# Performance work log

Measured on AMD Instinct MI355X. Metric: run time of the kernel, lower is better.

## Reference

```python
import jax, jax.numpy as jnp
import numpy as np

B, T, D_MODEL, HEAD_SIZE = 8, 1024, 1024, 64
BLOCK_SIZE = 1024  # == max_relative_pos


def setup_inputs() -> dict:
    key = jax.random.key(0)
    ks = jax.random.split(key, 7)
    s = 1.0 / np.sqrt(D_MODEL)
    return {
        "x": jax.random.normal(ks[0], (B, T, D_MODEL), dtype=jnp.float32),
        "Wk": jax.random.normal(ks[1], (D_MODEL, HEAD_SIZE), dtype=jnp.float32) * s,
        "bk": jax.random.normal(ks[2], (HEAD_SIZE,), dtype=jnp.float32) * 0.02,
        "Wq": jax.random.normal(ks[3], (D_MODEL, HEAD_SIZE), dtype=jnp.float32) * s,
        "bq": jax.random.normal(ks[4], (HEAD_SIZE,), dtype=jnp.float32) * 0.02,
        "Wv": jax.random.normal(ks[5], (D_MODEL, HEAD_SIZE), dtype=jnp.float32) * s,
        "rel_emb": jax.random.normal(ks[6], (2 * BLOCK_SIZE + 1, HEAD_SIZE), dtype=jnp.float32) * 0.02,
        "mask": 1,
    }


def reference(x, Wk, bk, Wq, bq, Wv, rel_emb, mask):
    Bb, Tt, _ = x.shape
    hs = Wk.shape[1]
    max_rel = (rel_emb.shape[0] - 1) // 2

    k = x @ Wk + bk          # [B,T,hs]
    q = x @ Wq + bq          # [B,T,hs]
    v = x @ Wv               # [B,T,hs]

    pos = jnp.arange(Tt)
    idx = jnp.clip(pos[:, None] - pos[None, :], -max_rel, max_rel) + max_rel
    r = rel_emb[idx]         # [T,T,hs], r[i,j] = emb(clip(i-j))

    # scores[b,i,j] = (q[b,i] + r[i,j]) . (k[b,j] + r[j,i]) / sqrt(hs)
    scale = 1.0 / np.sqrt(hs).astype(np.float32)
    scores = (
        jnp.einsum("bid,bjd->bij", q, k)
        + jnp.einsum("bid,jid->bij", q, r)   # q_i . r[j,i]
        + jnp.einsum("ijd,bjd->bij", r, k)   # r[i,j] . k_j
        + jnp.einsum("ijd,jid->ij", r, r)[None]  # r[i,j] . r[j,i]
    ) * scale

    if mask:  # static Python int -> causal mask, matches tril masked_fill
        causal = jnp.tril(jnp.ones((Tt, Tt), dtype=bool))
        scores = jnp.where(causal, scores, jnp.float32(-jnp.inf))

    w = jax.nn.softmax(scores, axis=-1)  # dropout is identity in eval mode
    return w @ v  # [B,T,hs]
```

## Files before the change

### kernel.cpp

```cpp
#include <hip/hip_runtime.h>
#include <hip/hip_bf16.h>
#include <math.h>


typedef __hip_bfloat16 bf16;
typedef __attribute__((ext_vector_type(8))) short short8;
typedef __attribute__((ext_vector_type(4))) float f32x4;

#define NTRI 136
#define MFMA16(a, b, c) __builtin_amdgcn_mfma_f32_16x16x32_bf16(a, b, c, 0, 0, 0)

__device__ __forceinline__ float bf2f(bf16 h) { return __bfloat162float(h); }
__device__ __forceinline__ bf16 f2bf(float f) { return __float2bfloat16(f); }
__device__ __forceinline__ short bfs(float f) {
  bf16 h = __float2bfloat16(f);
  return *(short*)&h;
}

union U16 {
  uint4 u;
  short8 s;
};
__device__ __forceinline__ short8 ldfrag(const bf16* p) {
  U16 x;
  x.u = *(const uint4*)p;
  return x.s;
}

__global__ __launch_bounds__(256) void prep_kernel(
    const float* __restrict__ Wk, const float* __restrict__ Wq, const float* __restrict__ Wv,
    const float* __restrict__ E, bf16* __restrict__ WT, bf16* __restrict__ Ep,
    bf16* __restrict__ Erev, float* __restrict__ rrG) {
  const int bid = blockIdx.x, t = threadIdx.x;
  if (bid < 768) {
    int idx = bid * 256 + t;
    int sel = idx >> 16, r = idx & 65535;
    int n = r >> 10, kk = r & 1023;
    const float* W = (sel == 0) ? Wk : (sel == 1) ? Wq : Wv;
    WT[idx] = f2bf(W[kk * 64 + n]);
  } else if (bid < 1281) {
    int idx = (bid - 768) * 256 + t;
    if (idx < 2049 * 64) {
      int tt = idx >> 6, d = idx & 63;
      Ep[idx] = f2bf(E[idx]);
      Erev[idx] = f2bf(E[(2048 - tt) * 64 + d]);
    }
  } else {
    int dlt = ((bid - 1281) << 2) + (t >> 6);
    int d = t & 63;
    float p = E[(size_t)(1024 + dlt) * 64 + d] * E[(size_t)(1024 - dlt) * 64 + d];
#pragma unroll
    for (int off = 32; off > 0; off >>= 1) p += __shfl_down(p, off);
    if (d == 0) rrG[64 + dlt] = p;
  }
}

__global__ __launch_bounds__(256, 2) void qkv_mfma(
    const float* __restrict__ x, const bf16* __restrict__ WT,
    const float* __restrict__ bk, const float* __restrict__ bq,
    bf16* __restrict__ qB, bf16* __restrict__ kB, bf16* __restrict__ vT) {
  const int R0 = blockIdx.x << 4;
  const int t = threadIdx.x;
  const int lane = t & 63, wave = t >> 6;
  const int m = lane & 15, quad = lane >> 4;

  __shared__ float RED[4][16][196];
  __shared__ bf16 VTS[64][24];

  const float* xrow = x + (size_t)(R0 + m) * 1024 + (wave << 8);
  f32x4 acc[3][4];
#pragma unroll
  for (int s = 0; s < 3; ++s)
#pragma unroll
    for (int c = 0; c < 4; ++c) acc[s][c] = (f32x4){0.f, 0.f, 0.f, 0.f};

#pragma unroll
  for (int ks = 0; ks < 8; ++ks) {
    const int k0 = ks * 32 + quad * 8;
    float4 xa = *(const float4*)(xrow + k0);
    float4 xb = *(const float4*)(xrow + k0 + 4);
    short8 a;
    a[0] = bfs(xa.x); a[1] = bfs(xa.y); a[2] = bfs(xa.z); a[3] = bfs(xa.w);
    a[4] = bfs(xb.x); a[5] = bfs(xb.y); a[6] = bfs(xb.z); a[7] = bfs(xb.w);
    const int kg = (wave << 8) + k0;
#pragma unroll
    for (int sel = 0; sel < 3; ++sel)
#pragma unroll
      for (int ct = 0; ct < 4; ++ct) {
        const bf16* bb = WT + ((size_t)(sel * 64 + ct * 16 + m) << 10) + kg;
        acc[sel][ct] = MFMA16(a, ldfrag(bb), acc[sel][ct]);
      }
  }

#pragma unroll
  for (int sel = 0; sel < 3; ++sel)
#pragma unroll
    for (int ct = 0; ct < 4; ++ct)
#pragma unroll
      for (int r = 0; r < 4; ++r)
        RED[wave][quad * 4 + r][sel * 64 + ct * 16 + m] = acc[sel][ct][r];
  __syncthreads();

#pragma unroll
  for (int e = 0; e < 12; ++e) {
    int idx = e * 256 + t;
    int row = idx / 192, c = idx - row * 192;
    float s = RED[0][row][c] + RED[1][row][c] + RED[2][row][c] + RED[3][row][c];
    int sel = c >> 6, col = c & 63;
    size_t grow = (size_t)(R0 + row);
    if (sel == 0) kB[grow * 64 + col] = f2bf(s + bk[col]);
    else if (sel == 1) qB[grow * 64 + col] = f2bf(s + bq[col]);
    else VTS[col][row] = f2bf(s);
  }
  __syncthreads();
  {
    int dd = t >> 2, h = (t & 3) << 2;
    int b = R0 >> 10, tloc = R0 & 1023;
    *(uint2*)(vT + ((size_t)((b << 6) + dd) << 10) + tloc + h) = *(const uint2*)&VTS[dd][h];
  }
}

__global__ __launch_bounds__(256, 3) void flash_mfma(
    const bf16* __restrict__ qB, const bf16* __restrict__ kB, const bf16* __restrict__ vT,
    const bf16* __restrict__ Ep, const bf16* __restrict__ Erev, const float* __restrict__ rrG,
    float* __restrict__ ml, float* __restrict__ Opart) {
  const int bx = blockIdx.x;
  const int b = bx / NTRI;
  const int rr_ = bx - b * NTRI;
  int it = (int)((sqrtf(8.f * rr_ + 1.f) - 1.f) * 0.5f);
  while ((it + 1) * (it + 2) / 2 <= rr_) ++it;
  while (it * (it + 1) / 2 > rr_) --it;
  const int jt = rr_ - it * (it + 1) / 2;
  const int I0 = it << 6, J0 = jt << 6;
  const int D = I0 - J0, w0 = D - 64;
  const int slot = bx;

  const int t = threadIdx.x;
  const int lane = t & 63, wave = t >> 6;
  const int m = lane & 15, quad = lane >> 4;
  const int strip = wave << 4;

  __shared__ __align__(16) bf16 M2S[64][136];
  __shared__ bf16 M3S[64][136];
  bf16 (*PS)[80] = (bf16(*)[80])M2S;

  const bf16* qbase = qB + ((size_t)((b << 10) + I0 + strip + m) << 6);
  const short8 aq0 = ldfrag(qbase + quad * 8);
  const short8 aq1 = ldfrag(qbase + 32 + quad * 8);
  const bf16* kbase = kB + ((size_t)((b << 10) + J0 + strip + m) << 6);
  const short8 ak0 = ldfrag(kbase + quad * 8);
  const short8 ak1 = ldfrag(kbase + 32 + quad * 8);

  const bf16* erb = Erev + ((size_t)(1024 + w0) << 6);
#pragma unroll
  for (int ct = 0; ct < 8; ++ct) {
    const bf16* bb = erb + ((size_t)(ct * 16 + m) << 6) + quad * 8;
    const float rv = rrG[64 + w0 + ct * 16 + m];
    f32x4 c = (f32x4){0.f, 0.f, 0.f, 0.f};
    c = MFMA16(aq0, ldfrag(bb), c);
    c = MFMA16(aq1, ldfrag(bb + 32), c);
#pragma unroll
    for (int r = 0; r < 4; ++r) M2S[strip + quad * 4 + r][ct * 16 + m] = f2bf(c[r] + rv);
  }
  const bf16* epb = Ep + ((size_t)(1024 + w0) << 6);
#pragma unroll
  for (int ct = 0; ct < 8; ++ct) {
    const bf16* bb = epb + ((size_t)(ct * 16 + m) << 6) + quad * 8;
    f32x4 c = (f32x4){0.f, 0.f, 0.f, 0.f};
    c = MFMA16(ak0, ldfrag(bb), c);
    c = MFMA16(ak1, ldfrag(bb + 32), c);
#pragma unroll
    for (int r = 0; r < 4; ++r) M3S[strip + quad * 4 + r][ct * 16 + m] = f2bf(c[r]);
  }
  f32x4 acc[4];
#pragma unroll
  for (int ct = 0; ct < 4; ++ct) {
    const bf16* bb = kB + ((size_t)((b << 10) + J0 + ct * 16 + m) << 6) + quad * 8;
    f32x4 c = (f32x4){0.f, 0.f, 0.f, 0.f};
    c = MFMA16(aq0, ldfrag(bb), c);
    c = MFMA16(aq1, ldfrag(bb + 32), c);
    acc[ct] = c;
  }
  __syncthreads();

  float sc[4][4], lrow[4] = {0.f, 0.f, 0.f, 0.f};
#pragma unroll
  for (int ct = 0; ct < 4; ++ct) {
    const int uj = ct * 16 + m;
#pragma unroll
    for (int r = 0; r < 4; ++r) {
      const int ui = strip + quad * 4 + r;
      float s;
      if (ui - uj + D >= 0) {
        const int wi = ui - uj + 64;
        s = (acc[ct][r] + bf2f(M2S[ui][wi]) + bf2f(M3S[uj][wi])) * 0.125f;
      } else {
        s = -INFINITY;
      }
      float p = __expf(s - 8.0f);
      sc[ct][r] = p;
      lrow[r] += p;
    }
  }
#pragma unroll
  for (int r = 0; r < 4; ++r) {
#pragma unroll
    for (int off = 1; off < 16; off <<= 1) lrow[r] += __shfl_xor(lrow[r], off);
  }
  if (m == 0) {
#pragma unroll
    for (int r = 0; r < 4; ++r)
      ml[(size_t)slot * 64 + strip + quad * 4 + r] = lrow[r];
  }
  __syncthreads();
#pragma unroll
  for (int ct = 0; ct < 4; ++ct)
#pragma unroll
    for (int r = 0; r < 4; ++r) PS[strip + quad * 4 + r][ct * 16 + m] = f2bf(sc[ct][r]);
  __syncthreads();

  const short8 ap0 = ldfrag(&PS[strip + m][quad * 8]);
  const short8 ap1 = ldfrag(&PS[strip + m][32 + quad * 8]);
  float* ob = Opart + (size_t)slot * 4096;
#pragma unroll
  for (int ct = 0; ct < 4; ++ct) {
    const bf16* bb = vT + ((size_t)(b * 64 + ct * 16 + m) << 10) + J0 + quad * 8;
    f32x4 o = (f32x4){0.f, 0.f, 0.f, 0.f};
    o = MFMA16(ap0, ldfrag(bb), o);
    o = MFMA16(ap1, ldfrag(bb + 32), o);
#pragma unroll
    for (int r = 0; r < 4; ++r)
      ob[(size_t)(strip + quad * 4 + r) * 64 + ct * 16 + m] = o[r];
  }
}

__global__ __launch_bounds__(256) void combine_kernel(
    const float* __restrict__ ml, const float* __restrict__ Opart, float* __restrict__ out) {
  const int row = (blockIdx.x << 2) + (threadIdx.x >> 6);
  const int d = threadIdx.x & 63;
  const int b = row >> 10, i = row & 1023;
  const int it = i >> 6, ii = i & 63;
  const int base = b * NTRI + it * (it + 1) / 2;

  float L = 0.f, O = 0.f;
  for (int jtt = 0; jtt <= it; ++jtt) {
    size_t slot = base + jtt;
    L += ml[slot * 64 + ii];
    O += Opart[slot * 4096 + (size_t)ii * 64 + d];
  }
  out[(size_t)row * 64 + d] = O / L;
}

extern "C" void kernel_launch(void* const* d_in, const int* in_sizes, int n_in,
                              void* d_out, int out_size, void* d_ws, size_t ws_size,
                              hipStream_t stream) {
  const float* x = (const float*)d_in[0];
  const float* Wk = (const float*)d_in[1];
  const float* bk = (const float*)d_in[2];
  const float* Wq = (const float*)d_in[3];
  const float* bq = (const float*)d_in[4];
  const float* Wv = (const float*)d_in[5];
  const float* E = (const float*)d_in[6];
  float* out = (float*)d_out;

  float* wsf = (float*)d_ws;
  float* ml = wsf;
  float* Opart = wsf + 69632;
  float* rrG = wsf + 69632 + 4456448;
  bf16* qB = (bf16*)(rrG + 1152);
  bf16* kB = qB + 524288;
  bf16* vT = kB + 524288;
  bf16* Ep = vT + 524288;
  bf16* Erev = Ep + 131200;
  bf16* WT = Erev + 131200;

  prep_kernel<<<1537, 256, 0, stream>>>(Wk, Wq, Wv, E, WT, Ep, Erev, rrG);
  qkv_mfma<<<512, 256, 0, stream>>>(x, WT, bk, bq, qB, kB, vT);
  flash_mfma<<<8 * NTRI, 256, 0, stream>>>(qB, kB, vT, Ep, Erev, rrG, ml, Opart);
  combine_kernel<<<2048, 256, 0, stream>>>(ml, Opart, out);
}
```

Before: 152.2 us.

## Replace per-tile partial outputs with atomic accumulation into final buffers

Each flash tile now atomically adds its unnormalized output and row sums straight into a shared per-row accumulator, instead of writing a separate partial slab per tile. A small normalize kernel then divides by the accumulated sum. This removes the roughly 17 MB partial-output write and the reduction reads in the combine step, at the cost of a memset and float atomic contention on hot rows (up to 16 tiles per row block). Floating-point summation order becomes nondeterministic.

After: 150.5 us. About the same (-1.1%).

```diff
diff --git a/kernel.cpp b/kernel.cpp
--- a/kernel.cpp
+++ b/kernel.cpp
@@ -123,7 +123,7 @@
 __global__ __launch_bounds__(256, 3) void flash_mfma(
     const bf16* __restrict__ qB, const bf16* __restrict__ kB, const bf16* __restrict__ vT,
     const bf16* __restrict__ Ep, const bf16* __restrict__ Erev, const float* __restrict__ rrG,
-    float* __restrict__ ml, float* __restrict__ Opart) {
+    float* __restrict__ Oacc, float* __restrict__ Lacc) {
   const int bx = blockIdx.x;
   const int b = bx / NTRI;
   const int rr_ = bx - b * NTRI;
@@ -133,7 +133,6 @@
   const int jt = rr_ - it * (it + 1) / 2;
   const int I0 = it << 6, J0 = jt << 6;
   const int D = I0 - J0, w0 = D - 64;
-  const int slot = bx;
 
   const int t = threadIdx.x;
   const int lane = t & 63, wave = t >> 6;
@@ -210,7 +209,7 @@
   if (m == 0) {
 #pragma unroll
     for (int r = 0; r < 4; ++r)
-      ml[(size_t)slot * 64 + strip + quad * 4 + r] = lrow[r];
+      atomicAdd(&Lacc[(b << 10) + I0 + strip + quad * 4 + r], lrow[r]);
   }
   __syncthreads();
 #pragma unroll
@@ -221,7 +220,7 @@
 
   const short8 ap0 = ldfrag(&PS[strip + m][quad * 8]);
   const short8 ap1 = ldfrag(&PS[strip + m][32 + quad * 8]);
-  float* ob = Opart + (size_t)slot * 4096;
+  float* ob = Oacc + ((size_t)((b << 10) + I0) << 6);
 #pragma unroll
   for (int ct = 0; ct < 4; ++ct) {
     const bf16* bb = vT + ((size_t)(b * 64 + ct * 16 + m) << 10) + J0 + quad * 8;
@@ -230,25 +229,14 @@
     o = MFMA16(ap1, ldfrag(bb + 32), o);
 #pragma unroll
     for (int r = 0; r < 4; ++r)
-      ob[(size_t)(strip + quad * 4 + r) * 64 + ct * 16 + m] = o[r];
-  }
-}
-
-__global__ __launch_bounds__(256) void combine_kernel(
-    const float* __restrict__ ml, const float* __restrict__ Opart, float* __restrict__ out) {
-  const int row = (blockIdx.x << 2) + (threadIdx.x >> 6);
-  const int d = threadIdx.x & 63;
-  const int b = row >> 10, i = row & 1023;
-  const int it = i >> 6, ii = i & 63;
-  const int base = b * NTRI + it * (it + 1) / 2;
-
-  float L = 0.f, O = 0.f;
-  for (int jtt = 0; jtt <= it; ++jtt) {
-    size_t slot = base + jtt;
-    L += ml[slot * 64 + ii];
-    O += Opart[slot * 4096 + (size_t)ii * 64 + d];
-  }
-  out[(size_t)row * 64 + d] = O / L;
+      atomicAdd(&ob[(size_t)(strip + quad * 4 + r) * 64 + ct * 16 + m], o[r]);
+  }
+}
+
+__global__ __launch_bounds__(256) void normalize_kernel(
+    const float* __restrict__ Oacc, const float* __restrict__ Lacc, float* __restrict__ out) {
+  int idx = blockIdx.x * 256 + threadIdx.x;
+  out[idx] = Oacc[idx] / Lacc[idx >> 6];
 }
 
 extern "C" void kernel_launch(void* const* d_in, const int* in_sizes, int n_in,
@@ -264,9 +252,9 @@
   float* out = (float*)d_out;
 
   float* wsf = (float*)d_ws;
-  float* ml = wsf;
-  float* Opart = wsf + 69632;
-  float* rrG = wsf + 69632 + 4456448;
+  float* Oacc = wsf;
+  float* Lacc = wsf + 524288;
+  float* rrG = wsf + 532480;
   bf16* qB = (bf16*)(rrG + 1152);
   bf16* kB = qB + 524288;
   bf16* vT = kB + 524288;
@@ -274,8 +262,9 @@
   bf16* Erev = Ep + 131200;
   bf16* WT = Erev + 131200;
 
+  hipMemsetAsync(Oacc, 0, (524288 + 8192) * sizeof(float), stream);
   prep_kernel<<<1537, 256, 0, stream>>>(Wk, Wq, Wv, E, WT, Ep, Erev, rrG);
   qkv_mfma<<<512, 256, 0, stream>>>(x, WT, bk, bq, qB, kB, vT);
-  flash_mfma<<<8 * NTRI, 256, 0, stream>>>(qB, kB, vT, Ep, Erev, rrG, ml, Opart);
-  combine_kernel<<<2048, 256, 0, stream>>>(ml, Opart, out);
-}
+  flash_mfma<<<8 * NTRI, 256, 0, stream>>>(qB, kB, vT, Ep, Erev, rrG, Oacc, Lacc);
+  normalize_kernel<<<2048, 256, 0, stream>>>(Oacc, Lacc, out);
+}
```
